# Kernel optimization log

Measured on AMD Instinct MI355X. Metric: run time of the kernel, lower is better.

Reference implementation:

```python
import jax, jax.numpy as jnp
import numpy as np

B, I, J, C = 1, 320, 320, 128
H, Dh = 4, 32
AH = H * Dh  # all_head_size == 128
EPS = 1e-5


def setup_inputs() -> dict:
    key = jax.random.key(0)
    ks = jax.random.split(key, 10)
    s = 0.05
    return {
        "z": jax.random.normal(ks[0], (B, I, J, C), jnp.float32),
        "z_mask": jax.random.randint(ks[1], (B, I, J), 0, 2, jnp.int32),
        "ln_scale": jnp.ones((C,), jnp.float32),
        "ln_bias": jnp.zeros((C,), jnp.float32),
        "Wq": jax.random.normal(ks[2], (C, AH), jnp.float32) * s,
        "Wk": jax.random.normal(ks[3], (C, AH), jnp.float32) * s,
        "Wv": jax.random.normal(ks[4], (C, AH), jnp.float32) * s,
        "Wg": jax.random.normal(ks[5], (C, AH), jnp.float32) * s,
        "bg": jnp.zeros((AH,), jnp.float32),
        "Wo": jax.random.normal(ks[6], (AH, C), jnp.float32) * s,
        "bo": jnp.zeros((C,), jnp.float32),
    }


def _layernorm(x, scale, bias):
    mu = jnp.mean(x, axis=-1, keepdims=True)
    var = jnp.var(x, axis=-1, keepdims=True)
    return (x - mu) * jax.lax.rsqrt(var + EPS) * scale + bias


def reference(z, z_mask, ln_scale, ln_bias, Wq, Wk, Wv, Wg, bg, Wo, bo):
    zn = _layernorm(z, ln_scale, ln_bias)                  # [B,I,J,C]
    m = z_mask.astype(jnp.float32)                         # [B,I,J]
    mask_bias = 1e9 * (m - 1.0)[:, :, None, None, :]       # [B,I,1,1,J]

    def heads(x):
        return x.reshape(x.shape[:-1] + (H, Dh))

    q = heads(zn @ Wq)                                     # [B,I,J,H,Dh]
    k = heads(zn @ Wk)
    v = heads(zn @ Wv)
    # NOTE: original module applies NO 1/sqrt(d) scaling — faithful.
    logits = jnp.einsum('biqhc,bikhc->bihqk', q, k) + mask_bias
    weights = jax.nn.softmax(logits, axis=-1)              # [B,I,H,J,J]
    wa = jnp.einsum('bihqk,bikhc->biqhc', weights, v)      # [B,I,J,H,Dh]
    g = jax.nn.sigmoid(heads(zn @ Wg + bg))                # [B,I,J,H,Dh]
    out = (g * wa).reshape(z.shape[:-1] + (AH,))           # [B,I,J,AH]
    return (out @ Wo + bo) * m[..., None]                  # [B,I,J,C]
```

## Files before the change

### kernel.cpp

```cpp
#include <hip/hip_runtime.h>

typedef _Float16 f16;
typedef _Float16 f16x2 __attribute__((ext_vector_type(2)));
typedef _Float16 f16x4 __attribute__((ext_vector_type(4)));
typedef _Float16 f16x8 __attribute__((ext_vector_type(8)));
typedef float f32x4 __attribute__((ext_vector_type(4)));

#define I_DIM 320
#define J_DIM 320
#define C_DIM 128
#define NROWS (I_DIM * J_DIM)
#define LOG2E 1.44269504f

__device__ inline float pkrtz(float a, float b) {
    return __builtin_bit_cast(float, __builtin_amdgcn_cvt_pkrtz(a, b));
}

__global__ __launch_bounds__(256) void prep_kernel(const float* __restrict__ Wq,
                                                   const float* __restrict__ Wk,
                                                   const float* __restrict__ Wv,
                                                   const float* __restrict__ Wg,
                                                   const float* __restrict__ Wo,
                                                   f16* __restrict__ Wfrag) {
    int f = blockIdx.x * 256 + threadIdx.x;
    int j = f & 7, lane = (f >> 3) & 63, n = (f >> 9) & 7;
    int ks = (f >> 12) & 3, w = f >> 14;
    int gq = lane >> 4, r16 = lane & 15;
    const float* W = (w == 0) ? Wq : (w == 1) ? Wk : (w == 2) ? Wv : (w == 3) ? Wg : Wo;
    float val = W[(size_t)(ks * 32 + gq * 8 + j) * 128 + n * 16 + r16];
    if (w == 0) val *= LOG2E;
    Wfrag[f] = (f16)val;
}

__global__ __launch_bounds__(256) void ln_kernel(const float* __restrict__ z,
                                                 const float* __restrict__ scale,
                                                 const float* __restrict__ bias,
                                                 f16* __restrict__ zn) {
    int wave = threadIdx.x >> 6;
    int lane = threadIdx.x & 63;
    int row = blockIdx.x * 4 + wave;
    const float* zr = z + (size_t)row * C_DIM;
    float2 x = *(const float2*)(zr + lane * 2);
    float s = x.x + x.y;
    float sq = x.x * x.x + x.y * x.y;
    #pragma unroll
    for (int o = 32; o; o >>= 1) {
        s  += __shfl_xor(s, o);
        sq += __shfl_xor(sq, o);
    }
    float mu = s * (1.0f / 128.0f);
    float var = sq * (1.0f / 128.0f) - mu * mu;
    float rs = rsqrtf(var + 1e-5f);
    int c0 = lane * 2;
    float y0 = (x.x - mu) * rs * scale[c0] + bias[c0];
    float y1 = (x.y - mu) * rs * scale[c0 + 1] + bias[c0 + 1];
    f16x2 o2 = {(f16)y0, (f16)y1};
    *(f16x2*)(zn + (size_t)row * C_DIM + c0) = o2;
}

__global__ __launch_bounds__(256, 3) void attn_mega(const f16* __restrict__ zn,
                                                    const f16* __restrict__ Wfrag,
                                                    const float* __restrict__ bg,
                                                    const int* __restrict__ z_mask,
                                                    f16* __restrict__ gwa) {
    __shared__ f16 Ksh[320][40];
    __shared__ f16 Vt[32][328];
    __shared__ float mbs[320];
    __shared__ f16 Pb[4][16][40];

    int bid = blockIdx.x;
    int xcd = bid & 7, idx = bid >> 3;
    int i = xcd * 40 + (idx >> 2);
    int h = idx & 3;
    size_t zbase = (size_t)i * (J_DIM * C_DIM);
    size_t gbase = zbase + h * 32;

    int wave = threadIdx.x >> 6;
    int lane = threadIdx.x & 63;
    int gq = lane >> 4, r16 = lane & 15;

    const f16* wfq = Wfrag;
    const f16* wfk = Wfrag + 16384;
    const f16* wfv = Wfrag + 32768;
    const f16* wfg = Wfrag + 49152;

    for (int t = threadIdx.x; t < 320; t += 256)
        mbs[t] = z_mask[i * J_DIM + t] ? -12.0f : -60000.0f;

    for (int rt = wave; rt < 20; rt += 4) {
        f16x8 a[4];
        #pragma unroll
        for (int ks = 0; ks < 4; ++ks)
            a[ks] = *(const f16x8*)(zn + zbase + (size_t)(rt * 16 + r16) * C_DIM + ks * 32 + gq * 8);
        f32x4 kacc[2] = {}, vacc[2] = {};
        #pragma unroll
        for (int ks = 0; ks < 4; ++ks) {
            #pragma unroll
            for (int n = 0; n < 2; ++n) {
                f16x8 bk = *(const f16x8*)(wfk + (ks * 8 + 2 * h + n) * 512 + lane * 8);
                kacc[n] = __builtin_amdgcn_mfma_f32_16x16x32_f16(a[ks], bk, kacc[n], 0, 0, 0);
                f16x8 bv = *(const f16x8*)(wfv + (ks * 8 + 2 * h + n) * 512 + lane * 8);
                vacc[n] = __builtin_amdgcn_mfma_f32_16x16x32_f16(a[ks], bv, vacc[n], 0, 0, 0);
            }
        }
        int colbase = (rt >> 1) * 32 + gq * 8 + (rt & 1) * 4;
        #pragma unroll
        for (int n = 0; n < 2; ++n) {
            #pragma unroll
            for (int rr = 0; rr < 4; ++rr)
                Ksh[rt * 16 + gq * 4 + rr][n * 16 + r16] = (f16)kacc[n][rr];
            f16x4 vp = {(f16)vacc[n][0], (f16)vacc[n][1], (f16)vacc[n][2], (f16)vacc[n][3]};
            *(f16x4*)(&Vt[n * 16 + r16][colbase]) = vp;
        }
    }
    __syncthreads();

    f16x8 qa[5];
    #pragma unroll
    for (int u = 0; u < 5; ++u) {
        int qt = u * 4 + wave;
        f16x8 a[4];
        #pragma unroll
        for (int ks = 0; ks < 4; ++ks)
            a[ks] = *(const f16x8*)(zn + zbase + (size_t)(qt * 16 + r16) * C_DIM + ks * 32 + gq * 8);
        f32x4 qacc[2] = {};
        #pragma unroll
        for (int ks = 0; ks < 4; ++ks) {
            #pragma unroll
            for (int n = 0; n < 2; ++n) {
                f16x8 bq = *(const f16x8*)(wfq + (ks * 8 + 2 * h + n) * 512 + lane * 8);
                qacc[n] = __builtin_amdgcn_mfma_f32_16x16x32_f16(a[ks], bq, qacc[n], 0, 0, 0);
            }
        }
        #pragma unroll
        for (int n = 0; n < 2; ++n)
            #pragma unroll
            for (int rr = 0; rr < 4; ++rr)
                Pb[wave][gq * 4 + rr][n * 16 + r16] = (f16)qacc[n][rr];
        asm volatile("s_waitcnt lgkmcnt(0)" ::: "memory");
        qa[u] = *(const f16x8*)(&Pb[wave][r16][gq * 8]);
    }

    const f16x8 ones = {(f16)1, (f16)1, (f16)1, (f16)1, (f16)1, (f16)1, (f16)1, (f16)1};
    f32x4 wa[5][2] = {};
    f32x4 wa2[5] = {};

    for (int kc = 0; kc < 10; ++kc) {
        f16x8 kb0 = *(const f16x8*)(&Ksh[kc * 32 + r16][gq * 8]);
        f16x8 kb1 = *(const f16x8*)(&Ksh[kc * 32 + 16 + r16][gq * 8]);
        f32x4 mk0 = *(const f32x4*)(&mbs[kc * 32 + 4 * gq]);
        f32x4 mk1 = *(const f32x4*)(&mbs[kc * 32 + 16 + 4 * gq]);
        f16x8 vb0 = *(const f16x8*)(&Vt[r16][kc * 32 + gq * 8]);
        f16x8 vb1 = *(const f16x8*)(&Vt[16 + r16][kc * 32 + gq * 8]);
        #pragma unroll
        for (int u = 0; u < 5; ++u) {
            f32x4 sc0 = __builtin_amdgcn_mfma_f32_16x16x32_f16(kb0, qa[u], mk0, 0, 0, 0);
            f32x4 sc1 = __builtin_amdgcn_mfma_f32_16x16x32_f16(kb1, qa[u], mk1, 0, 0, 0);
            float p0[4], p1[4];
            #pragma unroll
            for (int r = 0; r < 4; ++r) {
                p0[r] = __builtin_amdgcn_exp2f(sc0[r]);
                p1[r] = __builtin_amdgcn_exp2f(sc1[r]);
            }
            union { float f[4]; f16x8 v; } pu;
            pu.f[0] = pkrtz(p0[0], p0[1]);
            pu.f[1] = pkrtz(p0[2], p0[3]);
            pu.f[2] = pkrtz(p1[0], p1[1]);
            pu.f[3] = pkrtz(p1[2], p1[3]);
            wa[u][0] = __builtin_amdgcn_mfma_f32_16x16x32_f16(pu.v, vb0, wa[u][0], 0, 0, 0);
            wa[u][1] = __builtin_amdgcn_mfma_f32_16x16x32_f16(pu.v, vb1, wa[u][1], 0, 0, 0);
            wa2[u]   = __builtin_amdgcn_mfma_f32_16x16x32_f16(pu.v, ones, wa2[u], 0, 0, 0);
        }
    }

    float bgv0 = bg[h * 32 + r16];
    float bgv1 = bg[h * 32 + 16 + r16];
    #pragma unroll
    for (int u = 0; u < 5; ++u) {
        int qt = u * 4 + wave;
        float rinv[4];
        #pragma unroll
        for (int r = 0; r < 4; ++r)
            rinv[r] = 1.0f / wa2[u][r];
        f16x8 a[4];
        #pragma unroll
        for (int ks = 0; ks < 4; ++ks)
            a[ks] = *(const f16x8*)(zn + zbase + (size_t)(qt * 16 + r16) * C_DIM + ks * 32 + gq * 8);
        f32x4 gacc[2] = {};
        #pragma unroll
        for (int ks = 0; ks < 4; ++ks) {
            #pragma unroll
            for (int n = 0; n < 2; ++n) {
                f16x8 bgf = *(const f16x8*)(wfg + (ks * 8 + 2 * h + n) * 512 + lane * 8);
                gacc[n] = __builtin_amdgcn_mfma_f32_16x16x32_f16(a[ks], bgf, gacc[n], 0, 0, 0);
            }
        }
        #pragma unroll
        for (int n = 0; n < 2; ++n) {
            float bgn = n ? bgv1 : bgv0;
            #pragma unroll
            for (int r = 0; r < 4; ++r) {
                int jq = qt * 16 + gq * 4 + r;
                int dh = n * 16 + r16;
                float gv = 1.0f / (1.0f + __expf(-(gacc[n][r] + bgn)));
                gwa[gbase + (size_t)jq * C_DIM + dh] = (f16)(gv * wa[u][n][r] * rinv[r]);
            }
        }
    }
}

__global__ __launch_bounds__(256) void out_kernel(const f16* __restrict__ gwa,
                                                  const f16* __restrict__ Wofrag,
                                                  const float* __restrict__ bo,
                                                  const int* __restrict__ z_mask,
                                                  float* __restrict__ out) {
    int wave = threadIdx.x >> 6;
    int lane = threadIdx.x & 63;
    int gq = lane >> 4, r16 = lane & 15;
    int row0 = blockIdx.x * 256 + wave * 64;

    f32x4 acc[4][8] = {};
    #pragma unroll
    for (int ks = 0; ks < 4; ++ks) {
        f16x8 a[4];
        #pragma unroll
        for (int m = 0; m < 4; ++m)
            a[m] = *(const f16x8*)(gwa + (size_t)(row0 + m * 16 + r16) * C_DIM + ks * 32 + gq * 8);
        #pragma unroll
        for (int n = 0; n < 8; ++n) {
            f16x8 b = *(const f16x8*)(Wofrag + (ks * 8 + n) * 512 + lane * 8);
            #pragma unroll
            for (int m = 0; m < 4; ++m)
                acc[m][n] = __builtin_amdgcn_mfma_f32_16x16x32_f16(a[m], b, acc[m][n], 0, 0, 0);
        }
    }
    #pragma unroll
    for (int m = 0; m < 4; ++m) {
        #pragma unroll
        for (int rr = 0; rr < 4; ++rr) {
            int row = row0 + m * 16 + gq * 4 + rr;
            float mk = (float)z_mask[row];
            #pragma unroll
            for (int n = 0; n < 8; ++n) {
                int col = n * 16 + r16;
                out[(size_t)row * C_DIM + col] = (acc[m][n][rr] + bo[col]) * mk;
            }
        }
    }
}

extern "C" void kernel_launch(void* const* d_in, const int* in_sizes, int n_in,
                              void* d_out, int out_size, void* d_ws, size_t ws_size,
                              hipStream_t stream) {
    const float* z        = (const float*)d_in[0];
    const int*   z_mask   = (const int*)d_in[1];
    const float* ln_scale = (const float*)d_in[2];
    const float* ln_bias  = (const float*)d_in[3];
    const float* Wq       = (const float*)d_in[4];
    const float* Wk       = (const float*)d_in[5];
    const float* Wv       = (const float*)d_in[6];
    const float* Wg       = (const float*)d_in[7];
    const float* bg       = (const float*)d_in[8];
    const float* Wo       = (const float*)d_in[9];
    const float* bo       = (const float*)d_in[10];
    float* out = (float*)d_out;

    char* ws = (char*)d_ws;
    const size_t SZ = (size_t)NROWS * C_DIM * sizeof(f16);
    f16* zn    = (f16*)(ws);
    f16* gwa   = (f16*)(ws + 1 * SZ);
    f16* Wfrag = (f16*)(ws + 2 * SZ);

    prep_kernel<<<320, 256, 0, stream>>>(Wq, Wk, Wv, Wg, Wo, Wfrag);
    ln_kernel  <<<NROWS / 4, 256, 0, stream>>>(z, ln_scale, ln_bias, zn);
    attn_mega  <<<I_DIM * 4, 256, 0, stream>>>(zn, Wfrag, bg, z_mask, gwa);
    out_kernel <<<NROWS / 256, 256, 0, stream>>>(gwa, Wfrag + 4 * 16384, bo, z_mask, out);
}
```

Before: 110.0 us.

## Build Q fragments in registers via transposed MFMA and fuse gate projection

Q is now computed with swapped MFMA operands, so its accumulator can be packed directly into the B-operand fragment. This removes the LDS round trip through the Pb scratch buffer. To keep the QK^T dot product consistent, K is stored into shared memory with a permuted column order. The gate projection now runs in the same loop as Q, reusing the zn loads instead of reloading zn in the epilogue. The catch is ten extra live f32x4 accumulators across the attention loop, which raises register pressure at 3 waves per SIMD. The main loop also gets an unroll-by-2 hint.

```diff
diff --git a/kernel.cpp b/kernel.cpp
--- a/kernel.cpp
+++ b/kernel.cpp
@@ -66,7 +66,6 @@
     __shared__ f16 Ksh[320][40];
     __shared__ f16 Vt[32][328];
     __shared__ float mbs[320];
-    __shared__ f16 Pb[4][16][40];
 
     int bid = blockIdx.x;
     int xcd = bid & 7, idx = bid >> 3;
@@ -103,12 +102,13 @@
                 vacc[n] = __builtin_amdgcn_mfma_f32_16x16x32_f16(a[ks], bv, vacc[n], 0, 0, 0);
             }
         }
+        int kcol = (r16 >> 2) * 8 + (r16 & 3);
         int colbase = (rt >> 1) * 32 + gq * 8 + (rt & 1) * 4;
         #pragma unroll
         for (int n = 0; n < 2; ++n) {
             #pragma unroll
             for (int rr = 0; rr < 4; ++rr)
-                Ksh[rt * 16 + gq * 4 + rr][n * 16 + r16] = (f16)kacc[n][rr];
+                Ksh[rt * 16 + gq * 4 + rr][kcol + 4 * n] = (f16)kacc[n][rr];
             f16x4 vp = {(f16)vacc[n][0], (f16)vacc[n][1], (f16)vacc[n][2], (f16)vacc[n][3]};
             *(f16x4*)(&Vt[n * 16 + r16][colbase]) = vp;
         }
@@ -116,6 +116,7 @@
     __syncthreads();
 
     f16x8 qa[5];
+    f32x4 gacc[5][2] = {};
     #pragma unroll
     for (int u = 0; u < 5; ++u) {
         int qt = u * 4 + wave;
@@ -129,22 +130,24 @@
             #pragma unroll
             for (int n = 0; n < 2; ++n) {
                 f16x8 bq = *(const f16x8*)(wfq + (ks * 8 + 2 * h + n) * 512 + lane * 8);
-                qacc[n] = __builtin_amdgcn_mfma_f32_16x16x32_f16(a[ks], bq, qacc[n], 0, 0, 0);
-            }
-        }
-        #pragma unroll
-        for (int n = 0; n < 2; ++n)
-            #pragma unroll
-            for (int rr = 0; rr < 4; ++rr)
-                Pb[wave][gq * 4 + rr][n * 16 + r16] = (f16)qacc[n][rr];
-        asm volatile("s_waitcnt lgkmcnt(0)" ::: "memory");
-        qa[u] = *(const f16x8*)(&Pb[wave][r16][gq * 8]);
+                qacc[n] = __builtin_amdgcn_mfma_f32_16x16x32_f16(bq, a[ks], qacc[n], 0, 0, 0);
+                f16x8 bgf = *(const f16x8*)(wfg + (ks * 8 + 2 * h + n) * 512 + lane * 8);
+                gacc[u][n] = __builtin_amdgcn_mfma_f32_16x16x32_f16(a[ks], bgf, gacc[u][n], 0, 0, 0);
+            }
+        }
+        union { float f[4]; f16x8 v; } qu;
+        qu.f[0] = pkrtz(qacc[0][0], qacc[0][1]);
+        qu.f[1] = pkrtz(qacc[0][2], qacc[0][3]);
+        qu.f[2] = pkrtz(qacc[1][0], qacc[1][1]);
+        qu.f[3] = pkrtz(qacc[1][2], qacc[1][3]);
+        qa[u] = qu.v;
     }
 
     const f16x8 ones = {(f16)1, (f16)1, (f16)1, (f16)1, (f16)1, (f16)1, (f16)1, (f16)1};
     f32x4 wa[5][2] = {};
     f32x4 wa2[5] = {};
 
+    #pragma unroll 2
     for (int kc = 0; kc < 10; ++kc) {
         f16x8 kb0 = *(const f16x8*)(&Ksh[kc * 32 + r16][gq * 8]);
         f16x8 kb1 = *(const f16x8*)(&Ksh[kc * 32 + 16 + r16][gq * 8]);
@@ -182,19 +185,6 @@
         #pragma unroll
         for (int r = 0; r < 4; ++r)
             rinv[r] = 1.0f / wa2[u][r];
-        f16x8 a[4];
-        #pragma unroll
-        for (int ks = 0; ks < 4; ++ks)
-            a[ks] = *(const f16x8*)(zn + zbase + (size_t)(qt * 16 + r16) * C_DIM + ks * 32 + gq * 8);
-        f32x4 gacc[2] = {};
-        #pragma unroll
-        for (int ks = 0; ks < 4; ++ks) {
-            #pragma unroll
-            for (int n = 0; n < 2; ++n) {
-                f16x8 bgf = *(const f16x8*)(wfg + (ks * 8 + 2 * h + n) * 512 + lane * 8);
-                gacc[n] = __builtin_amdgcn_mfma_f32_16x16x32_f16(a[ks], bgf, gacc[n], 0, 0, 0);
-            }
-        }
         #pragma unroll
         for (int n = 0; n < 2; ++n) {
             float bgn = n ? bgv1 : bgv0;
@@ -202,7 +192,7 @@
             for (int r = 0; r < 4; ++r) {
                 int jq = qt * 16 + gq * 4 + r;
                 int dh = n * 16 + r16;
-                float gv = 1.0f / (1.0f + __expf(-(gacc[n][r] + bgn)));
+                float gv = 1.0f / (1.0f + __expf(-(gacc[u][n][r] + bgn)));
                 gwa[gbase + (size_t)jq * C_DIM + dh] = (f16)(gv * wa[u][n][r] * rinv[r]);
             }
         }
```

Result: faster. 97.82 us (-11.1%).
